# Performance work log

Hardware: AMD Instinct MI355X
Metric: run time of the kernel (lower is better)

## Reference

```python
import jax, jax.numpy as jnp
import numpy as np

N = 8192
K = 64
EPS = 1e-7
BN_EPS = 1e-5


def _norm(x):
    return jnp.sqrt(jnp.sum(x * x, axis=-1, keepdims=True))


def _bn(x, gamma, beta):
    # BatchNorm2d in training mode (batch statistics, biased variance)
    mu = jnp.mean(x, axis=(0, 2, 3), keepdims=True)
    var = jnp.mean((x - mu) ** 2, axis=(0, 2, 3), keepdims=True)
    return gamma.reshape(1, -1, 1, 1) * (x - mu) / jnp.sqrt(var + BN_EPS) + beta.reshape(1, -1, 1, 1)


def _conv1x1(x, w, b):
    # 1x1 conv == per-pixel linear: x [B,C,H,W], w [O,C]
    return jnp.einsum('bchw,oc->bohw', x, w) + b.reshape(1, -1, 1, 1)


def setup_inputs() -> dict:
    key = jax.random.key(0)
    ks = jax.random.split(key, 24)
    d = {}
    d['points'] = jax.random.normal(ks[0], (1, N, 3), jnp.float32)
    # graph_conv weights (torch code re-draws these every forward; here fixed params)
    lim0 = float(np.sqrt(6.0 / (4 + 64)))
    d['gw0'] = jax.random.uniform(ks[1], (4, 64), jnp.float32, -lim0, lim0)
    lim = float(np.sqrt(6.0 / (64 + 64)))
    for i in range(1, 5):
        d[f'gw{i}'] = jax.random.uniform(ks[1 + i], (64, 64), jnp.float32, -lim, lim)
    # mlp_1: 4->64->128, mlp_2: 192->256->1024 (1x1 convs + BN)
    d['c1w'] = jax.random.normal(ks[6], (64, 4), jnp.float32) * 0.1
    d['c1b'] = jnp.zeros((64,), jnp.float32)
    d['bn1g'] = jnp.ones((64,), jnp.float32)
    d['bn1b'] = jnp.zeros((64,), jnp.float32)
    d['c2w'] = jax.random.normal(ks[7], (128, 64), jnp.float32) * 0.1
    d['c2b'] = jnp.zeros((128,), jnp.float32)
    d['bn2g'] = jnp.ones((128,), jnp.float32)
    d['bn2b'] = jnp.zeros((128,), jnp.float32)
    d['c3w'] = jax.random.normal(ks[8], (256, 192), jnp.float32) * 0.05
    d['c3b'] = jnp.zeros((256,), jnp.float32)
    d['bn3g'] = jnp.ones((256,), jnp.float32)
    d['bn3b'] = jnp.zeros((256,), jnp.float32)
    d['c4w'] = jax.random.normal(ks[9], (1024, 256), jnp.float32) * 0.05
    d['c4b'] = jnp.zeros((1024,), jnp.float32)
    d['bn4g'] = jnp.ones((1024,), jnp.float32)
    d['bn4b'] = jnp.zeros((1024,), jnp.float32)
    return d


def _knn_search(points, k):
    # pairwise squared distances via ||a||^2 - 2ab + ||b||^2
    r = jnp.sum(points * points, axis=-1, keepdims=True)          # [1,N,1]
    dis = r - 2.0 * jnp.einsum('bnd,bmd->bnm', points, points) + jnp.swapaxes(r, 1, 2)
    _, idx = jax.lax.top_k(-dis, k)                                # [1,N,K]
    knn_pts = jax.vmap(lambda p, i: p[i])(points, idx)             # [1,N,K,3]
    return knn_pts


def _proj_knn(knn_pts):
    b, n, k, _ = knn_pts.shape
    pc = knn_pts - knn_pts[:, :, :1, :]                            # center on first neighbor (self)
    vn = jnp.sqrt(jnp.sum(pc * pc, axis=-1))                       # [1,N,K]
    id1 = jnp.argmax(vn, axis=-1)                                  # farthest neighbor
    a1 = jnp.take_along_axis(pc, jnp.broadcast_to(id1[:, :, None, None], (b, n, 1, 3)), axis=2)[:, :, 0, :]
    a1 = a1 / (_norm(a1) + EPS)
    a2 = jnp.mean(pc, axis=2)
    a2 = a2 / (_norm(a2) + EPS)
    a3 = a1 + 1.5 * a2
    a3 = a3 / (_norm(a3) + EPS)
    den = _norm(pc) + EPS                                          # [1,N,K,1]
    f1 = jnp.sum(pc * a1[:, :, None, :], axis=-1, keepdims=True) / den
    f2 = jnp.sum(pc * a2[:, :, None, :], axis=-1, keepdims=True) / den
    f3 = jnp.sum(pc * a3[:, :, None, :], axis=-1, keepdims=True) / den
    return jnp.concatenate([f1, f2, f3, vn[..., None]], axis=-1)   # [1,N,K,4]


def _proj_points(points):
    b, n, _ = points.shape
    vn = jnp.sqrt(jnp.sum(points * points, axis=-1))               # [1,N]
    i1 = jnp.argmax(vn, axis=-1)
    i2 = jnp.argmin(vn, axis=-1)
    a1 = jnp.take_along_axis(points, jnp.broadcast_to(i1[:, None, None], (b, 1, 3)), axis=1)[:, 0, :]
    a1 = a1 / (_norm(a1) + EPS)
    a2 = jnp.take_along_axis(points, jnp.broadcast_to(i2[:, None, None], (b, 1, 3)), axis=1)[:, 0, :]
    a2 = a2 / (_norm(a2) + EPS)
    a3 = a1 + 1.5 * a2
    a3 = a3 / (_norm(a3) + EPS)
    den = _norm(points) + EPS                                      # [1,N,1]
    f1 = jnp.sum(points * a1[:, None, :], axis=-1, keepdims=True) / den
    f2 = jnp.sum(points * a2[:, None, :], axis=-1, keepdims=True) / den
    f3 = jnp.sum(points * a3[:, None, :], axis=-1, keepdims=True) / den
    return jnp.concatenate([f1, f2, f3, vn[..., None]], axis=-1)   # [1,N,4]


def reference(points, gw0, gw1, gw2, gw3, gw4,
              c1w, c1b, bn1g, bn1b, c2w, c2b, bn2g, bn2b,
              c3w, c3b, bn3g, bn3b, c4w, c4b, bn4g, bn4b):
    n = points.shape[1]
    # upper branch: KNN -> rotation-invariant local feats -> 5-layer MLP -> max over K
    knn_pts = _knn_search(points, K)
    feat_up = _proj_knn(knn_pts)                                   # [1,N,K,4]
    x = feat_up.reshape(-1, 4)
    for w in (gw0, gw1, gw2, gw3, gw4):
        x = jax.nn.relu(x @ w)
    x = x.reshape(1, n, K, 64)
    emb_up = jnp.max(x, axis=2, keepdims=True)                     # [1,N,1,64]
    emb_up = emb_up.reshape(1, 64, n, 1)                           # raw view (reshape), as in torch
    # lower branch: global rotation-invariant feats -> mlp_1
    feat_down = _proj_points(points)                               # [1,N,4]
    emb_down = feat_down.reshape(1, 4, n, 1)                       # raw view (reshape), as in torch
    h = jax.nn.relu(_bn(_conv1x1(emb_down, c1w, c1b), bn1g, bn1b))
    h = jax.nn.relu(_bn(_conv1x1(h, c2w, c2b), bn2g, bn2b))        # [1,128,N,1]
    emb = jnp.concatenate([emb_up, h], axis=1)                     # [1,192,N,1]
    out = jax.nn.relu(_bn(_conv1x1(emb, c3w, c3b), bn3g, bn3b))
    out = jax.nn.relu(_bn(_conv1x1(out, c4w, c4b), bn4g, bn4b))    # [1,1024,N,1]
    return out
```

## Files before the change

### kernel.cpp

```cpp
#include <hip/hip_runtime.h>
#include <hip/hip_bf16.h>

#define NPTS 8192
#define KNN 64
#define EPSF 1e-7f

#define OFF_P4      0
#define OFF_STATS   32768
#define OFF_PART    36012
#define OFF_FEATDN  36864
#define OFF_WT1     69632
#define OFF_GWT     69888
#define OFF_BW2     79104
#define OFF_BW3     83200
#define OFF_BW4     107776
#define OFF_XB3V    238848
#define OFF_Y1      2336000
#define OFF_Y2      2860288
#define OFF_Y3      3908864
#define OFF_FEATUP  6006016

typedef __bf16 bf16x8 __attribute__((ext_vector_type(8)));
typedef float  f32x4  __attribute__((ext_vector_type(4)));

__device__ __forceinline__ unsigned f2u(float f) {
    unsigned u = __float_as_uint(f);
    return ((int)u >= 0) ? (u | 0x80000000u) : ~u;
}
__device__ __forceinline__ float key_to_f(unsigned long long k) {
    unsigned v = (unsigned)(k >> 32);
    unsigned ob = (v & 0x80000000u) ? (v ^ 0x80000000u) : ~v;
    return __uint_as_float(ob);
}
__device__ __forceinline__ unsigned short f2bf(float x) {
    union { __bf16 h; unsigned short s; } u;
    u.h = (__bf16)x;
    return u.s;
}
__device__ __forceinline__ unsigned packbf2(float lo, float hi) {
    return (unsigned)f2bf(lo) | ((unsigned)f2bf(hi) << 16);
}
__device__ __forceinline__ unsigned long long u64min(unsigned long long a, unsigned long long b){ return a < b ? a : b; }
__device__ __forceinline__ unsigned long long u64max(unsigned long long a, unsigned long long b){ return a < b ? b : a; }

__device__ __forceinline__ unsigned long long sort_merge(
    unsigned long long key, unsigned long long cur, int lane)
{
    #pragma unroll
    for (int k = 2; k <= 64; k <<= 1) {
        #pragma unroll
        for (int j = k >> 1; j > 0; j >>= 1) {
            unsigned long long o = __shfl_xor(key, j);
            bool up = ((lane & k) == 0);
            bool lower = ((lane & j) == 0);
            key = (lower == up) ? u64min(key, o) : u64max(key, o);
        }
    }
    unsigned long long rev = __shfl(key, 63 - lane);
    unsigned long long m = u64min(cur, rev);
    #pragma unroll
    for (int j = 32; j > 0; j >>= 1) {
        unsigned long long o = __shfl_xor(m, j);
        m = ((lane & j) == 0) ? u64min(m, o) : u64max(m, o);
    }
    return m;
}

__global__ __launch_bounds__(256) void prepwt_kernel(
    const float* __restrict__ points,
    const float* __restrict__ c1w, const float* __restrict__ c2w,
    const float* __restrict__ c3w, const float* __restrict__ c4w,
    const float* __restrict__ gw0, const float* __restrict__ gw1,
    const float* __restrict__ gw2, const float* __restrict__ gw3,
    const float* __restrict__ gw4,
    float* __restrict__ ws)
{
    const int t = blockIdx.x * 256 + threadIdx.x;
    const int T = 256 * 256;
    for (int m = t; m < 2944; m += T) ws[OFF_STATS + m] = 0.f;
    for (int m = t; m < 64*4; m += T) { int o = m >> 2, c = m & 3; ws[OFF_WT1 + c*64 + o] = c1w[m]; }

    unsigned short* bw2 = (unsigned short*)(ws + OFF_BW2);
    for (int m = t; m < 128*64; m += T)   bw2[m] = f2bf(c2w[m]);
    unsigned short* bw3 = (unsigned short*)(ws + OFF_BW3);
    for (int m = t; m < 256*192; m += T)  bw3[m] = f2bf(c3w[m]);
    unsigned short* bw4 = (unsigned short*)(ws + OFF_BW4);
    for (int m = t; m < 1024*256; m += T) bw4[m] = f2bf(c4w[m]);

    unsigned short* gwt = (unsigned short*)(ws + OFF_GWT);
    for (int m = t; m < 2048; m += T) {
        int o = m >> 5, i = m & 31;
        gwt[m] = (i < 4) ? f2bf(gw0[i*64 + o]) : (unsigned short)0;
    }
    const float* gsrc[4] = {gw1, gw2, gw3, gw4};
    for (int l = 0; l < 4; ++l) {
        const float* g = gsrc[l];
        unsigned short* dst = gwt + 2048 + l*4096;
        for (int m = t; m < 4096; m += T) { int o = m >> 6, i = m & 63; dst[m] = f2bf(g[i*64 + o]); }
    }

    if (blockIdx.x < 32) {
        const int n = blockIdx.x * 256 + threadIdx.x;
        float x = points[3*n+0], y = points[3*n+1], z = points[3*n+2];
        float rr = x*x + y*y + z*z;
        ((float4*)(ws + OFF_P4))[n] = make_float4(x, y, z, rr);
        float vn = sqrtf(rr);
        unsigned b = __float_as_uint(vn);
        unsigned long long mxk = ((unsigned long long)b << 32) | (unsigned long long)(0xFFFFFFFFu - (unsigned)n);
        unsigned long long mnk = ((unsigned long long)b << 32) | (unsigned long long)(unsigned)n;
        for (int j = 32; j > 0; j >>= 1) {
            mxk = u64max(mxk, __shfl_xor(mxk, j));
            mnk = u64min(mnk, __shfl_xor(mnk, j));
        }
        __shared__ unsigned long long smx[4], smn[4];
        int wid = threadIdx.x >> 6;
        if ((threadIdx.x & 63) == 0) { smx[wid] = mxk; smn[wid] = mnk; }
        __syncthreads();
        if (threadIdx.x == 0) {
            unsigned long long MX = 0ull, MN = ~0ull;
            for (int i = 0; i < 4; ++i) { MX = u64max(MX, smx[i]); MN = u64min(MN, smn[i]); }
            unsigned long long* parts = (unsigned long long*)(ws + OFF_PART);
            parts[2*blockIdx.x + 0] = MX;
            parts[2*blockIdx.x + 1] = MN;
        }
    }
}

__global__ __launch_bounds__(256) void prep_c_kernel(float* __restrict__ ws)
{
    __shared__ float av[9];
    const int tid = threadIdx.x;
    if (tid < 64) {
        const unsigned long long* parts = (const unsigned long long*)(ws + OFF_PART);
        unsigned long long mxk = (tid < 32) ? parts[2*tid + 0] : 0ull;
        unsigned long long mnk = (tid < 32) ? parts[2*tid + 1] : ~0ull;
        for (int j = 32; j > 0; j >>= 1) {
            mxk = u64max(mxk, __shfl_xor(mxk, j));
            mnk = u64min(mnk, __shfl_xor(mnk, j));
        }
        if (tid == 0) {
            int i1 = (int)(0xFFFFFFFFu - (unsigned)(mxk & 0xFFFFFFFFu));
            int i2 = (int)(unsigned)(mnk & 0xFFFFFFFFu);
            float4 p1 = ((const float4*)(ws + OFF_P4))[i1];
            float4 p2 = ((const float4*)(ws + OFF_P4))[i2];
            float n1 = sqrtf(p1.x*p1.x + p1.y*p1.y + p1.z*p1.z) + EPSF;
            float a1x = p1.x/n1, a1y = p1.y/n1, a1z = p1.z/n1;
            float n2 = sqrtf(p2.x*p2.x + p2.y*p2.y + p2.z*p2.z) + EPSF;
            float a2x = p2.x/n2, a2y = p2.y/n2, a2z = p2.z/n2;
            float a3x = a1x + 1.5f*a2x, a3y = a1y + 1.5f*a2y, a3z = a1z + 1.5f*a2z;
            float n3 = sqrtf(a3x*a3x + a3y*a3y + a3z*a3z) + EPSF;
            a3x /= n3; a3y /= n3; a3z /= n3;
            av[0]=a1x; av[1]=a1y; av[2]=a1z;
            av[3]=a2x; av[4]=a2y; av[5]=a2z;
            av[6]=a3x; av[7]=a3y; av[8]=a3z;
        }
    }
    __syncthreads();
    const int n = blockIdx.x * 256 + tid;
    float4 v = ((const float4*)(ws + OFF_P4))[n];
    float vn = sqrtf(v.w);
    float den = vn + EPSF;
    float f1 = (v.x*av[0] + v.y*av[1] + v.z*av[2]) / den;
    float f2 = (v.x*av[3] + v.y*av[4] + v.z*av[5]) / den;
    float f3 = (v.x*av[6] + v.y*av[7] + v.z*av[8]) / den;
    float4* f4 = (float4*)(ws + OFF_FEATDN + 4*n);
    *f4 = make_float4(f1, f2, f3, vn);
}

__global__ __launch_bounds__(512) void knn_feat_kernel(
    const float4* __restrict__ p4, float4* __restrict__ feat_up)
{
    __shared__ __align__(16) float4 scand[2048];
    __shared__ unsigned long long queue[8][128];
    const int lane = threadIdx.x & 63;
    const int wid  = threadIdx.x >> 6;
    const int q = blockIdx.x * 8 + wid;

    const float4 qa = p4[q];
    unsigned long long cur = ~0ull;
    float ke = __builtin_inff();
    int qc = 0;
    unsigned long long* Q = queue[wid];

    for (int base = 0; base < NPTS; base += 2048) {
        __syncthreads();
        for (int t = threadIdx.x; t < 2048; t += 512) scand[t] = p4[base + t];
        __syncthreads();
        #pragma unroll 2
        for (int sub = 0; sub < 2048; sub += 128) {
            float4 cd0 = scand[sub + lane];
            float4 cd1 = scand[sub + 64 + lane];
            float dot0 = fmaf(qa.x, cd0.x, fmaf(qa.y, cd0.y, qa.z * cd0.z));
            float dot1 = fmaf(qa.x, cd1.x, fmaf(qa.y, cd1.y, qa.z * cd1.z));
            float e0 = fmaf(-2.f, dot0, cd0.w);
            float e1 = fmaf(-2.f, dot1, cd1.w);
            bool p0 = e0 < ke;
            bool p1 = e1 < ke;
            unsigned long long m0 = __ballot(p0);
            unsigned long long m1 = __ballot(p1);
            if (m0) {
                int prefix = __builtin_amdgcn_mbcnt_hi((unsigned)(m0 >> 32),
                              __builtin_amdgcn_mbcnt_lo((unsigned)m0, 0));
                if (p0) Q[qc + prefix] = ((unsigned long long)f2u(e0) << 32)
                                       | (unsigned long long)(unsigned)(base + sub + lane);
                qc += __popcll(m0);
                if (qc >= 64) {
                    qc -= 64;
                    cur = sort_merge(Q[qc + lane], cur, lane);
                    ke = key_to_f(__shfl(cur, 63));
                }
            }
            if (m1) {
                int prefix = __builtin_amdgcn_mbcnt_hi((unsigned)(m1 >> 32),
                              __builtin_amdgcn_mbcnt_lo((unsigned)m1, 0));
                if (p1) Q[qc + prefix] = ((unsigned long long)f2u(e1) << 32)
                                       | (unsigned long long)(unsigned)(base + sub + 64 + lane);
                qc += __popcll(m1);
                if (qc >= 64) {
                    qc -= 64;
                    cur = sort_merge(Q[qc + lane], cur, lane);
                    ke = key_to_f(__shfl(cur, 63));
                }
            }
        }
    }
    cur = sort_merge((lane < qc) ? Q[lane] : ~0ull, cur, lane);

    int nidx = (int)(unsigned)(cur & 0xFFFFFFFFu);
    float4 np = p4[nidx];
    float ox = __shfl(np.x, 0), oy = __shfl(np.y, 0), oz = __shfl(np.z, 0);
    float pcx = np.x - ox, pcy = np.y - oy, pcz = np.z - oz;
    float vn = sqrtf(pcx*pcx + pcy*pcy + pcz*pcz);

    unsigned long long ak = ((unsigned long long)__float_as_uint(vn) << 32)
                          | (unsigned long long)(unsigned)(63 - lane);
    for (int s = 32; s > 0; s >>= 1) ak = u64max(ak, __shfl_xor(ak, s));
    int id1 = 63 - (int)(unsigned)(ak & 0xFFFFFFFFu);

    float a1x = __shfl(pcx, id1), a1y = __shfl(pcy, id1), a1z = __shfl(pcz, id1);
    float n1 = sqrtf(a1x*a1x + a1y*a1y + a1z*a1z) + EPSF;
    a1x /= n1; a1y /= n1; a1z /= n1;

    float sx = pcx, sy = pcy, sz = pcz;
    for (int s = 32; s > 0; s >>= 1) {
        sx += __shfl_xor(sx, s); sy += __shfl_xor(sy, s); sz += __shfl_xor(sz, s);
    }
    float a2x = sx * (1.f/64.f), a2y = sy * (1.f/64.f), a2z = sz * (1.f/64.f);
    float n2 = sqrtf(a2x*a2x + a2y*a2y + a2z*a2z) + EPSF;
    a2x /= n2; a2y /= n2; a2z /= n2;

    float a3x = a1x + 1.5f*a2x, a3y = a1y + 1.5f*a2y, a3z = a1z + 1.5f*a2z;
    float n3 = sqrtf(a3x*a3x + a3y*a3y + a3z*a3z) + EPSF;
    a3x /= n3; a3y /= n3; a3z /= n3;

    float den = vn + EPSF;
    float f1 = (pcx*a1x + pcy*a1y + pcz*a1z) / den;
    float f2 = (pcx*a2x + pcy*a2y + pcz*a2z) / den;
    float f3 = (pcx*a3x + pcy*a3y + pcz*a3z) / den;
    feat_up[q*64 + lane] = make_float4(f1, f2, f3, vn);
}

#define BROW 72
__global__ __launch_bounds__(256) void mlp_kernel(
    const float4* __restrict__ feat_up,
    const unsigned short* __restrict__ gwt,
    unsigned short* __restrict__ xb3v)
{
    __shared__ __align__(16) unsigned short Blds[4][64 * BROW];
    const int lane = threadIdx.x & 63;
    const int wid  = threadIdx.x >> 6;
    const int q = blockIdx.x * 4 + wid;
    const int c = lane & 15, g = lane >> 4;
    unsigned short* B = Blds[wid];

    {
        float4 f = feat_up[q*64 + lane];
        uint2 p0;
        p0.x = packbf2(f.x, f.y);
        p0.y = packbf2(f.z, f.w);
        *(uint2*)&B[lane*BROW] = p0;
        *(uint2*)&B[lane*BROW + 4] = make_uint2(0, 0);
        uint4 z4 = make_uint4(0, 0, 0, 0);
        *(uint4*)&B[lane*BROW + 8]  = z4;
        *(uint4*)&B[lane*BROW + 16] = z4;
        *(uint4*)&B[lane*BROW + 24] = z4;
    }

    const unsigned short* Wl[5] = {gwt, gwt + 2048, gwt + 6144, gwt + 10240, gwt + 14336};
    f32x4 acc[4][4];

    for (int layer = 0; layer < 5; ++layer) {
        const int wstride = (layer == 0) ? 32 : 64;
        const int nks = (layer == 0) ? 1 : 2;
        #pragma unroll
        for (int mb = 0; mb < 4; ++mb)
            #pragma unroll
            for (int nb = 0; nb < 4; ++nb)
                acc[mb][nb] = (f32x4){0.f, 0.f, 0.f, 0.f};

        for (int ks = 0; ks < nks; ++ks) {
            bf16x8 af[4], bf[4];
            #pragma unroll
            for (int mb = 0; mb < 4; ++mb)
                af[mb] = *(const bf16x8*)(Wl[layer] + (mb*16 + c)*wstride + ks*32 + g*8);
            #pragma unroll
            for (int nb = 0; nb < 4; ++nb)
                bf[nb] = *(const bf16x8*)&B[(nb*16 + c)*BROW + ks*32 + g*8];
            #pragma unroll
            for (int mb = 0; mb < 4; ++mb)
                #pragma unroll
                for (int nb = 0; nb < 4; ++nb)
                    acc[mb][nb] = __builtin_amdgcn_mfma_f32_16x16x32_bf16(af[mb], bf[nb], acc[mb][nb], 0, 0, 0);
        }

        if (layer < 4) {
            #pragma unroll
            for (int mb = 0; mb < 4; ++mb) {
                #pragma unroll
                for (int nb = 0; nb < 4; ++nb) {
                    f32x4 a = acc[mb][nb];
                    uint2 pw;
                    pw.x = packbf2(fmaxf(a[0], 0.f), fmaxf(a[1], 0.f));
                    pw.y = packbf2(fmaxf(a[2], 0.f), fmaxf(a[3], 0.f));
                    *(uint2*)&B[(nb*16 + c)*BROW + mb*16 + g*4] = pw;
                }
            }
        }
    }

    const int cc = q >> 7;
    const int pbase = (q & 127) << 6;
    #pragma unroll
    for (int mb = 0; mb < 4; ++mb) {
        float v[4];
        #pragma unroll
        for (int r = 0; r < 4; ++r)
            v[r] = fmaxf(fmaxf(fmaxf(acc[mb][0][r], acc[mb][1][r]),
                               fmaxf(acc[mb][2][r], acc[mb][3][r])), 0.f);
        #pragma unroll
        for (int mask = 1; mask <= 8; mask <<= 1)
            #pragma unroll
            for (int r = 0; r < 4; ++r)
                v[r] = fmaxf(v[r], __shfl_xor(v[r], mask));
        if (c == 0) {
            #pragma unroll
            for (int r = 0; r < 4; ++r) {
                const int f = mb*16 + g*4 + r;
                xb3v[(size_t)(pbase + f) * 64 + cc] = f2bf(v[r]);
            }
        }
    }
}

__global__ __launch_bounds__(256) void conv1_kernel(
    const float* __restrict__ x, const float* __restrict__ wt,
    const float* __restrict__ bias, float* __restrict__ y,
    float* __restrict__ stout)
{
    const int tid = threadIdx.x;
    const int p  = blockIdx.x * 256 + tid;
    const int o0 = blockIdx.y * 32;
    float acc[32];
    #pragma unroll
    for (int u = 0; u < 32; ++u) acc[u] = bias[o0 + u];
    #pragma unroll
    for (int c = 0; c < 4; ++c) {
        float xv = x[c * NPTS + p];
        const float* wr = wt + c * 64 + o0;
        #pragma unroll
        for (int u = 0; u < 32; ++u) acc[u] = fmaf(xv, wr[u], acc[u]);
    }
    #pragma unroll
    for (int u = 0; u < 32; ++u) y[(o0 + u) * NPTS + p] = acc[u];

    __shared__ float ps[4][32], pss[4][32];
    const int wid = tid >> 6, lane = tid & 63;
    #pragma unroll
    for (int u = 0; u < 32; ++u) {
        float s = acc[u], ss = acc[u] * acc[u];
        for (int j = 32; j > 0; j >>= 1) { s += __shfl_xor(s, j); ss += __shfl_xor(ss, j); }
        if (lane == 0) { ps[wid][u] = s; pss[wid][u] = ss; }
    }
    __syncthreads();
    if (tid < 32) {
        float S  = ps[0][tid] + ps[1][tid] + ps[2][tid] + ps[3][tid];
        float SS = pss[0][tid] + pss[1][tid] + pss[2][tid] + pss[3][tid];
        atomicAdd(&stout[o0 + tid], S);
        atomicAdd(&stout[64 + o0 + tid], SS);
    }
}

__global__ __launch_bounds__(256) void convbn_kernel(
    const unsigned short* __restrict__ A,
    const unsigned short* __restrict__ Bdir, int Kdir,
    const float* __restrict__ yprev,
    const float* __restrict__ stp, const float* __restrict__ gam, const float* __restrict__ bet,
    const float* __restrict__ bias, int K, int M,
    float* __restrict__ yout, float* __restrict__ stout)
{
    __shared__ float sc[256], sh[256];
    const int tid = threadIdx.x;
    const int Cp = K - Kdir;
    for (int cc = tid; cc < Cp; cc += 256) {
        float mu  = stp[cc] * (1.f / 8192.f);
        float var = stp[Cp + cc] * (1.f / 8192.f) - mu * mu;
        float s = gam[cc] / sqrtf(var + 1e-5f);
        sc[cc] = s; sh[cc] = bet[cc] - mu * s;
    }
    __syncthreads();

    const int lane = tid & 63;
    const int w = tid >> 6;
    const int n0 = blockIdx.x * 256 + w * 64;
    const int m0 = blockIdx.y * 64;
    const int c = lane & 15, g = lane >> 4;

    f32x4 acc[4][4];
    #pragma unroll
    for (int mt = 0; mt < 4; ++mt)
        #pragma unroll
        for (int nt = 0; nt < 4; ++nt)
            acc[mt][nt] = (f32x4){0.f, 0.f, 0.f, 0.f};

    for (int k0 = 0; k0 < K; k0 += 32) {
        bf16x8 af[4], bf[4];
        #pragma unroll
        for (int mt = 0; mt < 4; ++mt)
            af[mt] = *(const bf16x8*)(A + (size_t)(m0 + mt*16 + c) * K + k0 + g*8);
        if (k0 + 32 <= Kdir) {
            #pragma unroll
            for (int nt = 0; nt < 4; ++nt)
                bf[nt] = *(const bf16x8*)(Bdir + (size_t)(n0 + nt*16 + c) * Kdir + k0 + g*8);
        } else {
            const int ch0 = k0 - Kdir + g*8;
            #pragma unroll
            for (int nt = 0; nt < 4; ++nt) {
                const int pt = n0 + nt*16 + c;
                bf16x8 r;
                #pragma unroll
                for (int j = 0; j < 8; ++j) {
                    float vv = fmaxf(fmaf(yprev[(size_t)(ch0 + j) * NPTS + pt],
                                          sc[ch0 + j], sh[ch0 + j]), 0.f);
                    r[j] = (__bf16)vv;
                }
                bf[nt] = r;
            }
        }
        #pragma unroll
        for (int mt = 0; mt < 4; ++mt)
            #pragma unroll
            for (int nt = 0; nt < 4; ++nt)
                acc[mt][nt] = __builtin_amdgcn_mfma_f32_16x16x32_bf16(af[mt], bf[nt], acc[mt][nt], 0, 0, 0);
    }

    #pragma unroll
    for (int mt = 0; mt < 4; ++mt) {
        float s[4], ss[4];
        #pragma unroll
        for (int r = 0; r < 4; ++r) {
            const int o = m0 + mt*16 + g*4 + r;
            const float bv = bias[o];
            float sum = 0.f, sq = 0.f;
            #pragma unroll
            for (int nt = 0; nt < 4; ++nt) {
                float v = acc[mt][nt][r] + bv;
                yout[(size_t)o * NPTS + n0 + nt*16 + c] = v;
                sum += v; sq += v * v;
            }
            s[r] = sum; ss[r] = sq;
        }
        #pragma unroll
        for (int mask = 1; mask <= 8; mask <<= 1)
            #pragma unroll
            for (int r = 0; r < 4; ++r) {
                s[r]  += __shfl_xor(s[r],  mask);
                ss[r] += __shfl_xor(ss[r], mask);
            }
        if (c == 0) {
            #pragma unroll
            for (int r = 0; r < 4; ++r) {
                const int o = m0 + mt*16 + g*4 + r;
                atomicAdd(&stout[o], s[r]);
                atomicAdd(&stout[M + o], ss[r]);
            }
        }
    }
}

__global__ __launch_bounds__(256) void bnrelu_kernel(
    const float4* y, const float* __restrict__ st,
    const float* __restrict__ g, const float* __restrict__ b,
    float4* out, int C)
{
    int idx = blockIdx.x * 256 + threadIdx.x;
    int c = idx >> 11;
    float mu  = st[c] * (1.f / 8192.f);
    float var = st[C + c] * (1.f / 8192.f) - mu * mu;
    float scale = g[c] / sqrtf(var + 1e-5f);
    float sh = b[c] - mu * scale;
    float4 v = y[idx];
    v.x = fmaxf(fmaf(v.x, scale, sh), 0.f);
    v.y = fmaxf(fmaf(v.y, scale, sh), 0.f);
    v.z = fmaxf(fmaf(v.z, scale, sh), 0.f);
    v.w = fmaxf(fmaf(v.w, scale, sh), 0.f);
    out[idx] = v;
}

extern "C" void kernel_launch(void* const* d_in, const int* in_sizes, int n_in,
                              void* d_out, int out_size, void* d_ws, size_t ws_size,
                              hipStream_t stream) {
    const float* points = (const float*)d_in[0];
    const float* gw0 = (const float*)d_in[1];
    const float* gw1 = (const float*)d_in[2];
    const float* gw2 = (const float*)d_in[3];
    const float* gw3 = (const float*)d_in[4];
    const float* gw4 = (const float*)d_in[5];
    const float* c1w = (const float*)d_in[6];  const float* c1b = (const float*)d_in[7];
    const float* bn1g = (const float*)d_in[8]; const float* bn1b = (const float*)d_in[9];
    const float* c2w = (const float*)d_in[10]; const float* c2b = (const float*)d_in[11];
    const float* bn2g = (const float*)d_in[12];const float* bn2b = (const float*)d_in[13];
    const float* c3w = (const float*)d_in[14]; const float* c3b = (const float*)d_in[15];
    const float* bn3g = (const float*)d_in[16];const float* bn3b = (const float*)d_in[17];
    const float* c4w = (const float*)d_in[18]; const float* c4b = (const float*)d_in[19];
    const float* bn4g = (const float*)d_in[20];const float* bn4b = (const float*)d_in[21];

    float* ws = (float*)d_ws;
    float* p4f    = ws + OFF_P4;
    float* featdn = ws + OFF_FEATDN;
    float* featup = ws + OFF_FEATUP;
    float* y1 = ws + OFF_Y1; float* y2 = ws + OFF_Y2; float* y3 = ws + OFF_Y3;
    float* s1 = ws + OFF_STATS + 0;
    float* s2 = ws + OFF_STATS + 128;
    float* s3 = ws + OFF_STATS + 384;
    float* s4 = ws + OFF_STATS + 896;
    float* wt1 = ws + OFF_WT1;
    const unsigned short* gwt = (const unsigned short*)(ws + OFF_GWT);
    const unsigned short* bw2 = (const unsigned short*)(ws + OFF_BW2);
    const unsigned short* bw3 = (const unsigned short*)(ws + OFF_BW3);
    const unsigned short* bw4 = (const unsigned short*)(ws + OFF_BW4);
    unsigned short* xb3v = (unsigned short*)(ws + OFF_XB3V);
    float* outp = (float*)d_out;

    prepwt_kernel<<<256, 256, 0, stream>>>(points, c1w, c2w, c3w, c4w,
                                           gw0, gw1, gw2, gw3, gw4, ws);
    prep_c_kernel<<<32, 256, 0, stream>>>(ws);

    knn_feat_kernel<<<1024, 512, 0, stream>>>((const float4*)p4f, (float4*)featup);
    mlp_kernel<<<2048, 256, 0, stream>>>((const float4*)featup, gwt, xb3v);

    conv1_kernel<<<dim3(32, 2), 256, 0, stream>>>(featdn, wt1, c1b, y1, s1);
    convbn_kernel<<<dim3(32, 2), 256, 0, stream>>>(bw2, nullptr, 0, y1, s1, bn1g, bn1b,
                                                   c2b, 64, 128, y2, s2);
    convbn_kernel<<<dim3(32, 4), 256, 0, stream>>>(bw3, xb3v, 64, y2, s2, bn2g, bn2b,
                                                   c3b, 192, 256, y3, s3);
    convbn_kernel<<<dim3(32, 16), 256, 0, stream>>>(bw4, nullptr, 0, y3, s3, bn3g, bn3b,
                                                    c4b, 256, 1024, outp, s4);
    bnrelu_kernel<<<8192, 256, 0, stream>>>((const float4*)outp, s4, bn4g, bn4b, (float4*)outp, 1024);
}
```

Before: 332.8 us.

## Store intermediate conv activations point-major for vectorized loads and stores

The intermediate activations y1, y2 and y3 change from channel-major to point-major layout. Each thread can then read 8 consecutive channels with two float4 loads in the BN-on-load path and write its 4 outputs with one float4 store. conv1 now computes all 64 channels per thread in a single grid row, halving its block count. The final layer keeps channel-major output, and per-lane strided accesses across 64- to 256-float rows may reduce coalescing compared with the old layout.

```diff
diff --git a/kernel.cpp b/kernel.cpp
--- a/kernel.cpp
+++ b/kernel.cpp
@@ -359,34 +359,34 @@
 {
     const int tid = threadIdx.x;
     const int p  = blockIdx.x * 256 + tid;
-    const int o0 = blockIdx.y * 32;
-    float acc[32];
-    #pragma unroll
-    for (int u = 0; u < 32; ++u) acc[u] = bias[o0 + u];
+    float acc[64];
+    #pragma unroll
+    for (int u = 0; u < 64; ++u) acc[u] = bias[u];
     #pragma unroll
     for (int c = 0; c < 4; ++c) {
         float xv = x[c * NPTS + p];
-        const float* wr = wt + c * 64 + o0;
-        #pragma unroll
-        for (int u = 0; u < 32; ++u) acc[u] = fmaf(xv, wr[u], acc[u]);
-    }
-    #pragma unroll
-    for (int u = 0; u < 32; ++u) y[(o0 + u) * NPTS + p] = acc[u];
-
-    __shared__ float ps[4][32], pss[4][32];
+        const float* wr = wt + c * 64;
+        #pragma unroll
+        for (int u = 0; u < 64; ++u) acc[u] = fmaf(xv, wr[u], acc[u]);
+    }
+    #pragma unroll
+    for (int u = 0; u < 64; u += 4)
+        *(float4*)&y[(size_t)p * 64 + u] = make_float4(acc[u], acc[u+1], acc[u+2], acc[u+3]);
+
+    __shared__ float ps[4][64], pss[4][64];
     const int wid = tid >> 6, lane = tid & 63;
     #pragma unroll
-    for (int u = 0; u < 32; ++u) {
+    for (int u = 0; u < 64; ++u) {
         float s = acc[u], ss = acc[u] * acc[u];
         for (int j = 32; j > 0; j >>= 1) { s += __shfl_xor(s, j); ss += __shfl_xor(ss, j); }
         if (lane == 0) { ps[wid][u] = s; pss[wid][u] = ss; }
     }
     __syncthreads();
-    if (tid < 32) {
+    if (tid < 64) {
         float S  = ps[0][tid] + ps[1][tid] + ps[2][tid] + ps[3][tid];
         float SS = pss[0][tid] + pss[1][tid] + pss[2][tid] + pss[3][tid];
-        atomicAdd(&stout[o0 + tid], S);
-        atomicAdd(&stout[64 + o0 + tid], SS);
+        atomicAdd(&stout[tid], S);
+        atomicAdd(&stout[64 + tid], SS);
     }
 }
 
@@ -395,7 +395,7 @@
     const unsigned short* __restrict__ Bdir, int Kdir,
     const float* __restrict__ yprev,
     const float* __restrict__ stp, const float* __restrict__ gam, const float* __restrict__ bet,
-    const float* __restrict__ bias, int K, int M,
+    const float* __restrict__ bias, int K, int M, int outPM,
     float* __restrict__ yout, float* __restrict__ stout)
 {
     __shared__ float sc[256], sh[256];
@@ -433,16 +433,28 @@
                 bf[nt] = *(const bf16x8*)(Bdir + (size_t)(n0 + nt*16 + c) * Kdir + k0 + g*8);
         } else {
             const int ch0 = k0 - Kdir + g*8;
+            const float s0 = sc[ch0+0], h0 = sh[ch0+0];
+            const float s1 = sc[ch0+1], h1 = sh[ch0+1];
+            const float s2 = sc[ch0+2], h2 = sh[ch0+2];
+            const float s3 = sc[ch0+3], h3 = sh[ch0+3];
+            const float s4 = sc[ch0+4], h4 = sh[ch0+4];
+            const float s5 = sc[ch0+5], h5 = sh[ch0+5];
+            const float s6 = sc[ch0+6], h6 = sh[ch0+6];
+            const float s7 = sc[ch0+7], h7 = sh[ch0+7];
             #pragma unroll
             for (int nt = 0; nt < 4; ++nt) {
                 const int pt = n0 + nt*16 + c;
+                const float4 va = *(const float4*)&yprev[(size_t)pt * Cp + ch0];
+                const float4 vb = *(const float4*)&yprev[(size_t)pt * Cp + ch0 + 4];
                 bf16x8 r;
-                #pragma unroll
-                for (int j = 0; j < 8; ++j) {
-                    float vv = fmaxf(fmaf(yprev[(size_t)(ch0 + j) * NPTS + pt],
-                                          sc[ch0 + j], sh[ch0 + j]), 0.f);
-                    r[j] = (__bf16)vv;
-                }
+                r[0] = (__bf16)fmaxf(fmaf(va.x, s0, h0), 0.f);
+                r[1] = (__bf16)fmaxf(fmaf(va.y, s1, h1), 0.f);
+                r[2] = (__bf16)fmaxf(fmaf(va.z, s2, h2), 0.f);
+                r[3] = (__bf16)fmaxf(fmaf(va.w, s3, h3), 0.f);
+                r[4] = (__bf16)fmaxf(fmaf(vb.x, s4, h4), 0.f);
+                r[5] = (__bf16)fmaxf(fmaf(vb.y, s5, h5), 0.f);
+                r[6] = (__bf16)fmaxf(fmaf(vb.z, s6, h6), 0.f);
+                r[7] = (__bf16)fmaxf(fmaf(vb.w, s7, h7), 0.f);
                 bf[nt] = r;
             }
         }
@@ -455,19 +467,29 @@
 
     #pragma unroll
     for (int mt = 0; mt < 4; ++mt) {
-        float s[4], ss[4];
-        #pragma unroll
-        for (int r = 0; r < 4; ++r) {
-            const int o = m0 + mt*16 + g*4 + r;
-            const float bv = bias[o];
-            float sum = 0.f, sq = 0.f;
-            #pragma unroll
-            for (int nt = 0; nt < 4; ++nt) {
-                float v = acc[mt][nt][r] + bv;
-                yout[(size_t)o * NPTS + n0 + nt*16 + c] = v;
-                sum += v; sq += v * v;
-            }
-            s[r] = sum; ss[r] = sq;
+        const int ob = m0 + mt*16 + g*4;
+        const float4 bv4 = *(const float4*)&bias[ob];
+        float s[4] = {0.f, 0.f, 0.f, 0.f}, ss[4] = {0.f, 0.f, 0.f, 0.f};
+        #pragma unroll
+        for (int nt = 0; nt < 4; ++nt) {
+            float4 v;
+            v.x = acc[mt][nt][0] + bv4.x;
+            v.y = acc[mt][nt][1] + bv4.y;
+            v.z = acc[mt][nt][2] + bv4.z;
+            v.w = acc[mt][nt][3] + bv4.w;
+            const int pt = n0 + nt*16 + c;
+            if (outPM) {
+                *(float4*)&yout[(size_t)pt * M + ob] = v;
+            } else {
+                yout[(size_t)(ob+0) * NPTS + pt] = v.x;
+                yout[(size_t)(ob+1) * NPTS + pt] = v.y;
+                yout[(size_t)(ob+2) * NPTS + pt] = v.z;
+                yout[(size_t)(ob+3) * NPTS + pt] = v.w;
+            }
+            s[0] += v.x; ss[0] += v.x * v.x;
+            s[1] += v.y; ss[1] += v.y * v.y;
+            s[2] += v.z; ss[2] += v.z * v.z;
+            s[3] += v.w; ss[3] += v.w * v.w;
         }
         #pragma unroll
         for (int mask = 1; mask <= 8; mask <<= 1)
@@ -479,9 +501,8 @@
         if (c == 0) {
             #pragma unroll
             for (int r = 0; r < 4; ++r) {
-                const int o = m0 + mt*16 + g*4 + r;
-                atomicAdd(&stout[o], s[r]);
-                atomicAdd(&stout[M + o], ss[r]);
+                atomicAdd(&stout[ob + r], s[r]);
+                atomicAdd(&stout[M + ob + r], ss[r]);
             }
         }
     }
@@ -548,12 +569,12 @@
     knn_feat_kernel<<<1024, 512, 0, stream>>>((const float4*)p4f, (float4*)featup);
     mlp_kernel<<<2048, 256, 0, stream>>>((const float4*)featup, gwt, xb3v);
 
-    conv1_kernel<<<dim3(32, 2), 256, 0, stream>>>(featdn, wt1, c1b, y1, s1);
+    conv1_kernel<<<32, 256, 0, stream>>>(featdn, wt1, c1b, y1, s1);
     convbn_kernel<<<dim3(32, 2), 256, 0, stream>>>(bw2, nullptr, 0, y1, s1, bn1g, bn1b,
-                                                   c2b, 64, 128, y2, s2);
+                                                   c2b, 64, 128, 1, y2, s2);
     convbn_kernel<<<dim3(32, 4), 256, 0, stream>>>(bw3, xb3v, 64, y2, s2, bn2g, bn2b,
-                                                   c3b, 192, 256, y3, s3);
+                                                   c3b, 192, 256, 1, y3, s3);
     convbn_kernel<<<dim3(32, 16), 256, 0, stream>>>(bw4, nullptr, 0, y3, s3, bn3g, bn3b,
-                                                    c4b, 256, 1024, outp, s4);
+                                                    c4b, 256, 1024, 0, outp, s4);
     bnrelu_kernel<<<8192, 256, 0, stream>>>((const float4*)outp, s4, bn4g, bn4b, (float4*)outp, 1024);
 }
```

New measurement: 359.1 us. +7.9%, slower.
